# Kernel tuning notes

Hardware: AMD Instinct MI355X
Metric: run time of the kernel (lower is better)

## Reference

```python
import jax, jax.numpy as jnp
import numpy as np

B, S, HID = 2, 2048, 2048
NH, DN, DR, DV, RANK = 16, 128, 64, 128, 512
DQK = DN + DR
SCALE = DQK ** -0.5
EPS = 1e-5


def _rope(x, theta):
    # x: [..., d] with d even; theta broadcastable to [..., d//2] (angle per pair)
    x1, x2 = x[..., 0::2], x[..., 1::2]
    c, s = jnp.cos(theta), jnp.sin(theta)
    return jnp.stack([x1 * c - x2 * s, x1 * s + x2 * c], axis=-1).reshape(x.shape)


def _layernorm(x, gamma, beta):
    mu = jnp.mean(x, axis=-1, keepdims=True)
    var = jnp.var(x, axis=-1, keepdims=True)
    return (x - mu) * jax.lax.rsqrt(var + EPS) * gamma + beta


def setup_inputs() -> dict:
    key = jax.random.key(0)
    ks = jax.random.split(key, 8)
    def xavier(k, fan_in, fan_out, gain=1.0):
        lim = gain * np.sqrt(6.0 / (fan_in + fan_out))
        return jax.random.uniform(k, (fan_in, fan_out), jnp.float32, -lim, lim)
    return {
        "hidden_states": jax.random.normal(ks[0], (B, S, HID), jnp.float32),
        "freqs_cis": jax.random.uniform(ks[1], (S, DR // 2), jnp.float32) * 2.0 * np.pi,
        "Wq": xavier(ks[2], HID, NH * DQK),                      # q_proj (stored [in,out])
        "Wkv_a": xavier(ks[3], HID, RANK + DR),                  # kv_proj_a
        "kv_gamma": jnp.ones((RANK,), jnp.float32),              # kv_norm
        "kv_beta": jnp.zeros((RANK,), jnp.float32),
        "Wkv_b": xavier(ks[4], RANK, NH * (DN + DV)),            # kv_proj_b
        "Wout": xavier(ks[5], NH * DV, HID, gain=1.0 / np.sqrt(2.0)),  # out_proj
    }


def reference(hidden_states, freqs_cis, Wq, Wkv_a, kv_gamma, kv_beta, Wkv_b, Wout):
    b, s, _ = hidden_states.shape
    max_len = freqs_cis.shape[0]
    pos = jnp.arange(s) % max_len                      # [s], position_ids=None path
    theta = freqs_cis[pos]                             # [s, DR//2]

    # Q projection, split nope/rope, partial RoPE
    q = (hidden_states @ Wq).reshape(b, s, NH, DQK)
    q_nope, q_rope = q[..., :DN], q[..., DN:]
    q_rope = _rope(q_rope, theta[None, :, None, :])    # [b,s,nh,DR]

    # Low-rank KV: compressed latent + shared rope key
    kv = hidden_states @ Wkv_a                         # [b,s,RANK+DR]
    kv_c, k_rope = kv[..., :RANK], kv[..., RANK:]
    k_rope = _rope(k_rope, theta[None, :, :])          # [b,s,DR]
    kv_c = _layernorm(kv_c, kv_gamma, kv_beta)
    kvb = (kv_c @ Wkv_b).reshape(b, s, NH, DN + DV)
    k_nope, v = kvb[..., :DN], kvb[..., DN:]
    k = jnp.concatenate(
        [k_nope, jnp.broadcast_to(k_rope[:, :, None, :], (b, s, NH, DR))], axis=-1)

    q = jnp.concatenate([q_nope, q_rope], axis=-1)     # [b,s,nh,DQK]
    scores = jnp.einsum('bthd,bshd->btsh', q, k) * SCALE
    weights = jax.nn.softmax(scores.astype(jnp.float32), axis=2).astype(q.dtype)
    attn = jnp.einsum('btsh,bshd->bthd', weights, v).reshape(b, s, NH * DV)
    return attn @ Wout
```

## Files before the change

### kernel.cpp

```cpp
#include <hip/hip_runtime.h>

#define BATCH 2
#define SEQ   2048
#define HID   2048
#define NH    16
#define DN    128
#define DR    64
#define DV    128
#define RANK  512
#define DQK   192
#define NQ    (NH*DQK)
#define NKVA  576
#define NKVAP 640
#define NKVB  (NH*(DN+DV))
#define NTOK  (BATCH*SEQ)
#define SCALE_F 0.07216878364870323f

typedef __bf16 bf16x8 __attribute__((ext_vector_type(8)));
typedef float  f32x4  __attribute__((ext_vector_type(4)));
typedef unsigned int u32x4 __attribute__((ext_vector_type(4)));
typedef unsigned short u16;
typedef unsigned short u16x4 __attribute__((ext_vector_type(4)));

__device__ __forceinline__ float b2f(u16 h) {
    unsigned int u = ((unsigned int)h) << 16;
    float f; __builtin_memcpy(&f, &u, 4); return f;
}
__device__ __forceinline__ u16 f2b(float f) {
    unsigned int x; __builtin_memcpy(&x, &f, 4);
    unsigned int r = x + 0x7fffu + ((x >> 16) & 1u);
    return (u16)(r >> 16);
}
__device__ __forceinline__ bf16x8 lds_frag(const u16* p) {
    u32x4 v = *(const u32x4*)p;
    return __builtin_bit_cast(bf16x8, v);
}
__device__ __forceinline__ bf16x8 to_frag(u32x4 v) {
    return __builtin_bit_cast(bf16x8, v);
}
__device__ __forceinline__ f32x4 mfma16(bf16x8 a, bf16x8 b, f32x4 c) {
    return __builtin_amdgcn_mfma_f32_16x16x32_bf16(a, b, c, 0, 0, 0);
}
__device__ __forceinline__ void store_out(u16* p, float v) { *p = f2b(v); }
__device__ __forceinline__ void store_out(float* p, float v) { *p = v; }
__device__ __forceinline__ void gld_lds16(const u16* g, u16* l) {
    __builtin_amdgcn_global_load_lds(
        (const __attribute__((address_space(1))) unsigned int*)g,
        (__attribute__((address_space(3))) unsigned int*)l, 16, 0, 0);
}

__global__ void cast_f32_bf16(const float* __restrict__ in, u16* __restrict__ out, int n4) {
    int i = blockIdx.x * blockDim.x + threadIdx.x;
    if (i >= n4) return;
    f32x4 v = *(const f32x4*)(in + (size_t)i * 4);
    u16 o[4];
    for (int k = 0; k < 4; k++) o[k] = f2b(v[k]);
    *(unsigned long long*)(out + (size_t)i * 4) = *(unsigned long long*)o;
}

__global__ void transpose_pad(const float* __restrict__ in, u16* __restrict__ out,
                              int R, int C, int Cp) {
    __shared__ unsigned int t32[64 * 65];
    int r0 = blockIdx.x * 64, c0 = blockIdx.y * 64;
    int tid = threadIdx.x;
    bool valid = (c0 < C);
    for (int i = 0; i < 4; i++) {
        int u = tid + i * 256;
        int rl = u >> 4, c4 = u & 15;
        f32x4 v = {0.f, 0.f, 0.f, 0.f};
        if (valid) v = *(const f32x4*)&in[(size_t)(r0 + rl) * C + c0 + c4 * 4];
        for (int j = 0; j < 4; j++)
            t32[(c4 * 4 + j) * 65 + rl] = f2b(v[j]);
    }
    __syncthreads();
    for (int i = 0; i < 2; i++) {
        int u = tid + i * 256;
        int cl = u >> 3, r8 = (u & 7) * 8;
        unsigned int w[8];
        for (int j = 0; j < 8; j++) w[j] = t32[cl * 65 + r8 + j];
        u32x4 pk;
        for (int j = 0; j < 4; j++) pk[j] = (w[2 * j] & 0xffffu) | (w[2 * j + 1] << 16);
        *(u32x4*)&out[(size_t)(c0 + cl) * R + r0 + r8] = pk;
    }
}

template <typename OutT>
__global__ __launch_bounds__(256) void gemm_bt(const u16* __restrict__ A,
                                               const u16* __restrict__ Bt,
                                               OutT* __restrict__ C,
                                               int K, int lda, int ldb, int ldc) {
    __shared__ u16 As[128 * 32];
    __shared__ u16 Bs[128 * 32];
    int tid = threadIdx.x, lane = tid & 63, w = tid >> 6;
    int wm = (w >> 1) * 64, wn = (w & 1) * 64;
    int g = lane >> 4, ln = lane & 15;
    int m0 = blockIdx.y * 128, n0 = blockIdx.x * 128;
    f32x4 acc[4][4] = {};
    for (int k0 = 0; k0 < K; k0 += 32) {
        for (int i = 0; i < 2; i++) {
            int ch = tid + i * 256;
            int row = ch >> 2, o = ch & 3;
            gld_lds16(&A[(size_t)(m0 + row) * lda + k0 + o * 8], &As[row * 32 + o * 8]);
            gld_lds16(&Bt[(size_t)(n0 + row) * ldb + k0 + o * 8], &Bs[row * 32 + o * 8]);
        }
        __syncthreads();
        bf16x8 af[4], bf[4];
        for (int i = 0; i < 4; i++) af[i] = lds_frag(&As[(wm + i * 16 + ln) * 32 + g * 8]);
        for (int j = 0; j < 4; j++) bf[j] = lds_frag(&Bs[(wn + j * 16 + ln) * 32 + g * 8]);
        for (int i = 0; i < 4; i++)
            for (int j = 0; j < 4; j++)
                acc[i][j] = mfma16(af[i], bf[j], acc[i][j]);
        __syncthreads();
    }
    for (int i = 0; i < 4; i++)
        for (int j = 0; j < 4; j++)
            for (int r = 0; r < 4; r++) {
                int m = m0 + wm + i * 16 + g * 4 + r;
                int n = n0 + wn + j * 16 + ln;
                store_out(&C[(size_t)m * ldc + n], acc[i][j][r]);
            }
}

__global__ void rope_q(u16* __restrict__ q, const float* __restrict__ freqs) {
    int token = blockIdx.x;
    int s = token & (SEQ - 1);
    int tid = threadIdx.x;
    for (int i = 0; i < 2; i++) {
        int idx = tid + i * 256;
        int hh = idx >> 5, p = idx & 31;
        float th = freqs[s * 32 + p];
        float c = __cosf(th), sn = __sinf(th);
        size_t off = (size_t)token * NQ + hh * DQK + DN + 2 * p;
        float x1 = b2f(q[off]), x2 = b2f(q[off + 1]);
        q[off]     = f2b(x1 * c - x2 * sn);
        q[off + 1] = f2b(x1 * sn + x2 * c);
    }
}

__global__ void ln_kv(const u16* __restrict__ kvraw, const float* __restrict__ gamma,
                      const float* __restrict__ beta, u16* __restrict__ kv_c) {
    int row = blockIdx.x, tid = threadIdx.x;
    size_t base = (size_t)row * NKVAP;
    float x0 = b2f(kvraw[base + tid]), x1 = b2f(kvraw[base + 256 + tid]);
    float s = x0 + x1, q2 = x0 * x0 + x1 * x1;
    for (int o = 32; o > 0; o >>= 1) { s += __shfl_xor(s, o); q2 += __shfl_xor(q2, o); }
    __shared__ float sh[8];
    int lane = tid & 63, w = tid >> 6;
    if (lane == 0) { sh[w] = s; sh[4 + w] = q2; }
    __syncthreads();
    float S = sh[0] + sh[1] + sh[2] + sh[3];
    float Q2 = sh[4] + sh[5] + sh[6] + sh[7];
    float mu = S * (1.f / 512.f);
    float var = Q2 * (1.f / 512.f) - mu * mu;
    float rs = rsqrtf(var + 1e-5f);
    kv_c[(size_t)row * RANK + tid] =
        f2b((x0 - mu) * rs * gamma[tid] + beta[tid]);
    kv_c[(size_t)row * RANK + 256 + tid] =
        f2b((x1 - mu) * rs * gamma[256 + tid] + beta[256 + tid]);
}

__global__ void k_assemble(const u16* __restrict__ kvb, const u16* __restrict__ kvraw,
                           const float* __restrict__ freqs, u16* __restrict__ Kf) {
    int token = blockIdx.x;
    int s = token & (SEQ - 1);
    int tid = threadIdx.x;
    __shared__ u16 roped[64];
    if (tid < 32) {
        int p = tid;
        float th = freqs[s * 32 + p];
        float c = __cosf(th), sn = __sinf(th);
        float x1 = b2f(kvraw[(size_t)token * NKVAP + RANK + 2 * p]);
        float x2 = b2f(kvraw[(size_t)token * NKVAP + RANK + 2 * p + 1]);
        roped[2 * p]     = f2b(x1 * c - x2 * sn);
        roped[2 * p + 1] = f2b(x1 * sn + x2 * c);
    }
    __syncthreads();
    {
        int hh = tid >> 4, d8 = (tid & 15) * 8;
        *(u32x4*)&Kf[(size_t)token * NQ + hh * DQK + d8] =
            *(const u32x4*)&kvb[(size_t)token * NKVB + hh * 256 + d8];
    }
    if (tid < 128) {
        int hh = tid >> 3, d8 = (tid & 7) * 8;
        *(u32x4*)&Kf[(size_t)token * NQ + hh * DQK + DN + d8] = *(u32x4*)&roped[d8];
    }
}

__global__ void v_transpose(const u16* __restrict__ kvb, u16* __restrict__ Vt) {
    __shared__ unsigned int t32[64 * 65];
    int st = blockIdx.x * 64, dt = blockIdx.y * 64;
    int b = blockIdx.z >> 4, h = blockIdx.z & 15;
    int tid = threadIdx.x;
    for (int i = 0; i < 2; i++) {
        int u = tid + i * 256;
        int sl = u >> 3, c8 = (u & 7) * 8;
        u32x4 v = *(const u32x4*)&kvb[((size_t)(b * SEQ + st + sl) * NH + h) * 256 + DN + dt + c8];
        for (int j = 0; j < 4; j++) {
            t32[(c8 + 2 * j) * 65 + sl]     = v[j] & 0xffffu;
            t32[(c8 + 2 * j + 1) * 65 + sl] = v[j] >> 16;
        }
    }
    __syncthreads();
    for (int i = 0; i < 2; i++) {
        int u = tid + i * 256;
        int dl = u >> 3, s8 = (u & 7) * 8;
        unsigned int w[8];
        for (int j = 0; j < 8; j++) w[j] = t32[dl * 65 + s8 + j];
        u32x4 pk;
        for (int j = 0; j < 4; j++) pk[j] = (w[2 * j] & 0xffffu) | (w[2 * j + 1] << 16);
        *(u32x4*)&Vt[((size_t)(b * NH + h) * DV + dt + dl) * SEQ + st + s8] = pk;
    }
}

#define KC    64
#define QTILE 64
#define QSTR 200
#define PSTR 72
#define VSTR 72
#define NIT  (SEQ / KC)
__global__ __launch_bounds__(256, 3) void attn_kernel(const u16* __restrict__ Q,
                                                      const u16* __restrict__ Kf,
                                                      const u16* __restrict__ Vt,
                                                      u16* __restrict__ O) {
    __shared__ u16 Ks[KC * QSTR];
    __shared__ u16 Ps[QTILE * PSTR];
    __shared__ u16 Vs[DV * VSTR];
    __shared__ float lsumLDS[2][QTILE];
    int tid = threadIdx.x, lane = tid & 63, w = tid >> 6;
    int w1 = w & 1;
    int w2 = w >> 1;
    int g = lane >> 4, ln = lane & 15;
    int qt = blockIdx.x, h = blockIdx.y, b = blockIdx.z;

    size_t qbase  = ((size_t)(b * SEQ + qt * QTILE) * NH + h) * DQK;
    size_t kbase0 = ((size_t)(b * SEQ) * NH + h) * DQK;
    size_t vbase  = (size_t)(b * NH + h) * DV * SEQ;

    bf16x8 bfq[2][6];
    for (int ni = 0; ni < 2; ni++)
        for (int kk = 0; kk < 6; kk++)
            bfq[ni][kk] = to_frag(*(const u32x4*)&Q[qbase +
                (size_t)(w1 * 32 + ni * 16 + ln) * NQ + kk * 32 + g * 8]);

    u32x4 kpre[6], vpre[4];
    {
        int krow = tid >> 2;
        for (int i = 0; i < 6; i++) {
            int o = (tid & 3) + 4 * i;
            kpre[i] = *(const u32x4*)&Kf[kbase0 + (size_t)krow * NQ + o * 8];
        }
        int vrow = tid >> 1;
        for (int i = 0; i < 4; i++) {
            int o = (tid & 1) + 2 * i;
            vpre[i] = *(const u32x4*)&Vt[vbase + (size_t)vrow * SEQ + o * 8];
        }
    }
    f32x4 oacc[2][4] = {};
    float lpriv[2] = {0.f, 0.f};

    for (int kt = 0; kt < NIT; kt++) {
        {
            int krow = tid >> 2;
            for (int i = 0; i < 6; i++) {
                int o = (tid & 3) + 4 * i;
                *(u32x4*)&Ks[krow * QSTR + o * 8] = kpre[i];
            }
            int vrow = tid >> 1;
            for (int i = 0; i < 4; i++) {
                int o = (tid & 1) + 2 * i;
                *(u32x4*)&Vs[vrow * VSTR + o * 8] = vpre[i];
            }
        }
        __syncthreads();
        if (kt + 1 < NIT) {
            size_t kb = kbase0 + (size_t)(kt + 1) * KC * NQ;
            int krow = tid >> 2;
            for (int i = 0; i < 6; i++) {
                int o = (tid & 3) + 4 * i;
                kpre[i] = *(const u32x4*)&Kf[kb + (size_t)krow * NQ + o * 8];
            }
            int vrow = tid >> 1;
            int c0 = (kt + 1) * KC;
            for (int i = 0; i < 4; i++) {
                int o = (tid & 1) + 2 * i;
                vpre[i] = *(const u32x4*)&Vt[vbase + (size_t)vrow * SEQ + c0 + o * 8];
            }
        }
        f32x4 sacc[2][2] = {};
        for (int kk = 0; kk < 6; kk++) {
            bf16x8 af[2];
            for (int mi = 0; mi < 2; mi++)
                af[mi] = lds_frag(&Ks[(w2 * 32 + mi * 16 + ln) * QSTR + kk * 32 + g * 8]);
            for (int mi = 0; mi < 2; mi++)
                for (int ni = 0; ni < 2; ni++)
                    sacc[mi][ni] = mfma16(af[mi], bfq[ni][kk], sacc[mi][ni]);
        }
        for (int mi = 0; mi < 2; mi++)
            for (int ni = 0; ni < 2; ni++) {
                float p0 = __expf(sacc[mi][ni][0] * SCALE_F);
                float p1 = __expf(sacc[mi][ni][1] * SCALE_F);
                float p2 = __expf(sacc[mi][ni][2] * SCALE_F);
                float p3 = __expf(sacc[mi][ni][3] * SCALE_F);
                lpriv[ni] += (p0 + p1) + (p2 + p3);
                u16x4 pk = { f2b(p0), f2b(p1), f2b(p2), f2b(p3) };
                *(u16x4*)&Ps[(w1 * 32 + ni * 16 + ln) * PSTR + (w2 * 32 + mi * 16 + g * 4)] = pk;
            }
        __syncthreads();
        for (int kk = 0; kk < 2; kk++) {
            bf16x8 pa[2], vb[4];
            for (int mi = 0; mi < 2; mi++)
                pa[mi] = lds_frag(&Ps[(w1 * 32 + mi * 16 + ln) * PSTR + kk * 32 + g * 8]);
            for (int ni = 0; ni < 4; ni++)
                vb[ni] = lds_frag(&Vs[(w2 * 64 + ni * 16 + ln) * VSTR + kk * 32 + g * 8]);
            for (int mi = 0; mi < 2; mi++)
                for (int ni = 0; ni < 4; ni++)
                    oacc[mi][ni] = mfma16(pa[mi], vb[ni], oacc[mi][ni]);
        }
        __syncthreads();
    }

    for (int ni = 0; ni < 2; ni++) {
        float v = lpriv[ni];
        v += __shfl_xor(v, 16);
        v += __shfl_xor(v, 32);
        if (g == 0) lsumLDS[w2][w1 * 32 + ni * 16 + ln] = v;
    }
    __syncthreads();
    for (int mi = 0; mi < 2; mi++)
        for (int ni = 0; ni < 4; ni++) {
            int d = w2 * 64 + ni * 16 + ln;
            for (int r = 0; r < 4; r++) {
                int row = w1 * 32 + mi * 16 + g * 4 + r;
                float l = lsumLDS[0][row] + lsumLDS[1][row];
                O[((size_t)(b * SEQ + qt * QTILE + row) * NH + h) * DV + d] =
                    f2b(oacc[mi][ni][r] / l);
            }
        }
}

extern "C" void kernel_launch(void* const* d_in, const int* in_sizes, int n_in,
                              void* d_out, int out_size, void* d_ws, size_t ws_size,
                              hipStream_t stream) {
    const float* hs_f  = (const float*)d_in[0];
    const float* freqs = (const float*)d_in[1];
    const float* Wq    = (const float*)d_in[2];
    const float* Wkva  = (const float*)d_in[3];
    const float* gamma = (const float*)d_in[4];
    const float* beta  = (const float*)d_in[5];
    const float* Wkvb  = (const float*)d_in[6];
    const float* Wout  = (const float*)d_in[7];
    float* outp = (float*)d_out;

    char* ws = (char*)d_ws;
    size_t off = 0;
    auto alloc = [&](size_t elems) -> u16* {
        u16* p = (u16*)(ws + off);
        off += ((elems * 2 + 255) / 256) * 256;
        return p;
    };
    u16* hs    = alloc((size_t)NTOK * HID);
    u16* WqT   = alloc((size_t)NQ * HID);
    u16* WkvaT = alloc((size_t)NKVAP * HID);
    u16* WkvbT = alloc((size_t)NKVB * RANK);
    u16* WoutT = alloc((size_t)HID * HID);
    u16* q_raw = alloc((size_t)NTOK * NQ);
    u16* kvraw = alloc((size_t)NTOK * NKVAP);
    u16* kv_c  = alloc((size_t)NTOK * RANK);
    u16* kvb   = alloc((size_t)NTOK * NKVB);
    u16* Kf    = alloc((size_t)NTOK * NQ);
    u16* Vt    = alloc((size_t)BATCH * NH * DV * SEQ);
    u16* attn  = alloc((size_t)NTOK * NH * DV);
    (void)ws_size; (void)in_sizes; (void)n_in; (void)out_size;

    cast_f32_bf16<<<(NTOK * HID / 4 + 255) / 256, 256, 0, stream>>>(hs_f, hs, NTOK * HID / 4);
    transpose_pad<<<dim3(HID / 64, NQ / 64), 256, 0, stream>>>(Wq, WqT, HID, NQ, NQ);
    transpose_pad<<<dim3(HID / 64, NKVAP / 64), 256, 0, stream>>>(Wkva, WkvaT, HID, NKVA, NKVAP);
    transpose_pad<<<dim3(RANK / 64, NKVB / 64), 256, 0, stream>>>(Wkvb, WkvbT, RANK, NKVB, NKVB);
    transpose_pad<<<dim3(HID / 64, HID / 64), 256, 0, stream>>>(Wout, WoutT, HID, HID, HID);

    gemm_bt<<<dim3(NQ / 128, NTOK / 128), 256, 0, stream>>>(hs, WqT, q_raw, HID, HID, HID, NQ);
    rope_q<<<NTOK, 256, 0, stream>>>(q_raw, freqs);

    gemm_bt<<<dim3(NKVAP / 128, NTOK / 128), 256, 0, stream>>>(hs, WkvaT, kvraw, HID, HID, HID, NKVAP);
    ln_kv<<<NTOK, 256, 0, stream>>>(kvraw, gamma, beta, kv_c);

    gemm_bt<<<dim3(NKVB / 128, NTOK / 128), 256, 0, stream>>>(kv_c, WkvbT, kvb, RANK, RANK, RANK, NKVB);

    k_assemble<<<NTOK, 256, 0, stream>>>(kvb, kvraw, freqs, Kf);
    v_transpose<<<dim3(SEQ / 64, DV / 64, BATCH * NH), 256, 0, stream>>>(kvb, Vt);

    attn_kernel<<<dim3(SEQ / QTILE, NH, BATCH), 256, 0, stream>>>(q_raw, Kf, Vt, attn);

    gemm_bt<<<dim3(HID / 128, NTOK / 128), 256, 0, stream>>>(attn, WoutT, outp, HID, HID, HID, HID);
}
```

Measured before the change: 495.6 us.

## Load K via direct global-to-LDS, read V straight from global, raise occupancy

The attention kernel no longer stages K and V through registers. K tiles are copied with direct global-to-LDS loads into a fragment-ordered layout, and V fragments are read straight from global memory into registers, so the V LDS buffer and one barrier per iteration go away. Launch bounds rise from 3 to 4 blocks per CU because LDS and register use drop. In exchange, the register-level prefetch of the next tile is gone, so global load latency is less hidden. The direct LDS load issued after the last barrier also relies on the P·V phase and the next barrier for ordering, which may be racy with the Ks reads.

```diff
diff --git a/kernel.cpp b/kernel.cpp
--- a/kernel.cpp
+++ b/kernel.cpp
@@ -214,17 +214,14 @@
 
 #define KC    64
 #define QTILE 64
-#define QSTR 200
-#define PSTR 72
-#define VSTR 72
+#define PSTR  72
 #define NIT  (SEQ / KC)
-__global__ __launch_bounds__(256, 3) void attn_kernel(const u16* __restrict__ Q,
+__global__ __launch_bounds__(256, 4) void attn_kernel(const u16* __restrict__ Q,
                                                       const u16* __restrict__ Kf,
                                                       const u16* __restrict__ Vt,
                                                       u16* __restrict__ O) {
-    __shared__ u16 Ks[KC * QSTR];
+    __shared__ u16 Ks[24 * 64 * 8];
     __shared__ u16 Ps[QTILE * PSTR];
-    __shared__ u16 Vs[DV * VSTR];
     __shared__ float lsumLDS[2][QTILE];
     int tid = threadIdx.x, lane = tid & 63, w = tid >> 6;
     int w1 = w & 1;
@@ -242,55 +239,23 @@
             bfq[ni][kk] = to_frag(*(const u32x4*)&Q[qbase +
                 (size_t)(w1 * 32 + ni * 16 + ln) * NQ + kk * 32 + g * 8]);
 
-    u32x4 kpre[6], vpre[4];
-    {
-        int krow = tid >> 2;
-        for (int i = 0; i < 6; i++) {
-            int o = (tid & 3) + 4 * i;
-            kpre[i] = *(const u32x4*)&Kf[kbase0 + (size_t)krow * NQ + o * 8];
-        }
-        int vrow = tid >> 1;
-        for (int i = 0; i < 4; i++) {
-            int o = (tid & 1) + 2 * i;
-            vpre[i] = *(const u32x4*)&Vt[vbase + (size_t)vrow * SEQ + o * 8];
-        }
-    }
     f32x4 oacc[2][4] = {};
     float lpriv[2] = {0.f, 0.f};
 
     for (int kt = 0; kt < NIT; kt++) {
-        {
-            int krow = tid >> 2;
-            for (int i = 0; i < 6; i++) {
-                int o = (tid & 3) + 4 * i;
-                *(u32x4*)&Ks[krow * QSTR + o * 8] = kpre[i];
-            }
-            int vrow = tid >> 1;
-            for (int i = 0; i < 4; i++) {
-                int o = (tid & 1) + 2 * i;
-                *(u32x4*)&Vs[vrow * VSTR + o * 8] = vpre[i];
-            }
+        size_t kb = kbase0 + (size_t)kt * KC * NQ;
+        for (int i = 0; i < 6; i++) {
+            int c = tid + i * 256;
+            int r = c & 63, j = c >> 6;
+            gld_lds16(&Kf[kb + (size_t)r * NQ + j * 8], &Ks[c * 8]);
         }
         __syncthreads();
-        if (kt + 1 < NIT) {
-            size_t kb = kbase0 + (size_t)(kt + 1) * KC * NQ;
-            int krow = tid >> 2;
-            for (int i = 0; i < 6; i++) {
-                int o = (tid & 3) + 4 * i;
-                kpre[i] = *(const u32x4*)&Kf[kb + (size_t)krow * NQ + o * 8];
-            }
-            int vrow = tid >> 1;
-            int c0 = (kt + 1) * KC;
-            for (int i = 0; i < 4; i++) {
-                int o = (tid & 1) + 2 * i;
-                vpre[i] = *(const u32x4*)&Vt[vbase + (size_t)vrow * SEQ + c0 + o * 8];
-            }
-        }
+
         f32x4 sacc[2][2] = {};
         for (int kk = 0; kk < 6; kk++) {
             bf16x8 af[2];
             for (int mi = 0; mi < 2; mi++)
-                af[mi] = lds_frag(&Ks[(w2 * 32 + mi * 16 + ln) * QSTR + kk * 32 + g * 8]);
+                af[mi] = lds_frag(&Ks[(((kk * 4 + g) << 6) + w2 * 32 + mi * 16 + ln) * 8]);
             for (int mi = 0; mi < 2; mi++)
                 for (int ni = 0; ni < 2; ni++)
                     sacc[mi][ni] = mfma16(af[mi], bfq[ni][kk], sacc[mi][ni]);
@@ -305,18 +270,24 @@
                 u16x4 pk = { f2b(p0), f2b(p1), f2b(p2), f2b(p3) };
                 *(u16x4*)&Ps[(w1 * 32 + ni * 16 + ln) * PSTR + (w2 * 32 + mi * 16 + g * 4)] = pk;
             }
+        u32x4 vb[2][4];
+        {
+            int c0 = kt * KC;
+            for (int kk = 0; kk < 2; kk++)
+                for (int ni = 0; ni < 4; ni++)
+                    vb[kk][ni] = *(const u32x4*)&Vt[vbase +
+                        (size_t)(w2 * 64 + ni * 16 + ln) * SEQ + c0 + kk * 32 + g * 8];
+        }
         __syncthreads();
+
         for (int kk = 0; kk < 2; kk++) {
-            bf16x8 pa[2], vb[4];
+            bf16x8 pa[2];
             for (int mi = 0; mi < 2; mi++)
                 pa[mi] = lds_frag(&Ps[(w1 * 32 + mi * 16 + ln) * PSTR + kk * 32 + g * 8]);
-            for (int ni = 0; ni < 4; ni++)
-                vb[ni] = lds_frag(&Vs[(w2 * 64 + ni * 16 + ln) * VSTR + kk * 32 + g * 8]);
             for (int mi = 0; mi < 2; mi++)
                 for (int ni = 0; ni < 4; ni++)
-                    oacc[mi][ni] = mfma16(pa[mi], vb[ni], oacc[mi][ni]);
-        }
-        __syncthreads();
+                    oacc[mi][ni] = mfma16(pa[mi], to_frag(vb[kk][ni]), oacc[mi][ni]);
+        }
     }
 
     for (int ni = 0; ni < 2; ni++) {
```

After: 735.7 us. 1.48x slower.

## Fuse Q and KV-A projections into one GEMM and merge prep kernels

Applied to the files above, without the earlier changes.

Concatenates the transposed Wq and Wkv_a weights into a single 3712-column matrix so the Q projection and the compressed-KV projection run as one GEMM over the hidden states. The separate cast and four transpose launches are also folded into one prep kernel that dispatches by block index. Downstream kernels (rope_q, ln_kv, k_assemble, attention) now read from the combined qkv buffer with the new row stride. This is meant to cut launch overhead, read the hidden states once instead of twice, and fill the GPU better with one larger GEMM grid. The trade-off is that Q rows are no longer contiguous for the attention kernel's loads.

```diff
diff --git a/kernel.cpp b/kernel.cpp
--- a/kernel.cpp
+++ b/kernel.cpp
@@ -10,8 +10,7 @@
 #define RANK  512
 #define DQK   192
 #define NQ    (NH*DQK)
-#define NKVA  576
-#define NKVAP 640
+#define NQKV  3712
 #define NKVB  (NH*(DN+DV))
 #define NTOK  (BATCH*SEQ)
 #define SCALE_F 0.07216878364870323f
@@ -49,20 +48,29 @@
         (__attribute__((address_space(3))) unsigned int*)l, 16, 0, 0);
 }
 
-__global__ void cast_f32_bf16(const float* __restrict__ in, u16* __restrict__ out, int n4) {
-    int i = blockIdx.x * blockDim.x + threadIdx.x;
-    if (i >= n4) return;
-    f32x4 v = *(const f32x4*)(in + (size_t)i * 4);
-    u16 o[4];
-    for (int k = 0; k < 4; k++) o[k] = f2b(v[k]);
-    *(unsigned long long*)(out + (size_t)i * 4) = *(unsigned long long*)o;
-}
-
-__global__ void transpose_pad(const float* __restrict__ in, u16* __restrict__ out,
-                              int R, int C, int Cp) {
+__global__ __launch_bounds__(256) void prep_kernel(
+        const float* __restrict__ hs_f, u16* __restrict__ hs,
+        const float* __restrict__ Wq, const float* __restrict__ Wkva,
+        const float* __restrict__ Wkvb, const float* __restrict__ Wout,
+        u16* __restrict__ WqkvT, u16* __restrict__ WkvbT, u16* __restrict__ WoutT) {
+    int tid = threadIdx.x;
+    int bid = blockIdx.x;
+    if (bid < 8192) {
+        int i = bid * 256 + tid;
+        f32x4 v = *(const f32x4*)(hs_f + (size_t)i * 4);
+        u16 o[4];
+        for (int k = 0; k < 4; k++) o[k] = f2b(v[k]);
+        *(unsigned long long*)(hs + (size_t)i * 4) = *(unsigned long long*)o;
+        return;
+    }
+    bid -= 8192;
+    const float* in; u16* out; int R, C, tilesC;
+    if (bid < 1536)      { in = Wq;   out = WqkvT;                       R = HID;  C = NQ;   tilesC = 48; }
+    else if (bid < 1856) { bid -= 1536; in = Wkva; out = WqkvT + (size_t)NQ * HID; R = HID; C = 576; tilesC = 10; }
+    else if (bid < 2368) { bid -= 1856; in = Wkvb; out = WkvbT;          R = RANK; C = NKVB; tilesC = 64; }
+    else                 { bid -= 2368; in = Wout; out = WoutT;          R = HID;  C = HID;  tilesC = 32; }
     __shared__ unsigned int t32[64 * 65];
-    int r0 = blockIdx.x * 64, c0 = blockIdx.y * 64;
-    int tid = threadIdx.x;
+    int r0 = (bid / tilesC) * 64, c0 = (bid % tilesC) * 64;
     bool valid = (c0 < C);
     for (int i = 0; i < 4; i++) {
         int u = tid + i * 256;
@@ -121,7 +129,7 @@
             }
 }
 
-__global__ void rope_q(u16* __restrict__ q, const float* __restrict__ freqs) {
+__global__ void rope_q(u16* __restrict__ qkv, const float* __restrict__ freqs) {
     int token = blockIdx.x;
     int s = token & (SEQ - 1);
     int tid = threadIdx.x;
@@ -130,18 +138,18 @@
         int hh = idx >> 5, p = idx & 31;
         float th = freqs[s * 32 + p];
         float c = __cosf(th), sn = __sinf(th);
-        size_t off = (size_t)token * NQ + hh * DQK + DN + 2 * p;
-        float x1 = b2f(q[off]), x2 = b2f(q[off + 1]);
-        q[off]     = f2b(x1 * c - x2 * sn);
-        q[off + 1] = f2b(x1 * sn + x2 * c);
-    }
-}
-
-__global__ void ln_kv(const u16* __restrict__ kvraw, const float* __restrict__ gamma,
+        size_t off = (size_t)token * NQKV + hh * DQK + DN + 2 * p;
+        float x1 = b2f(qkv[off]), x2 = b2f(qkv[off + 1]);
+        qkv[off]     = f2b(x1 * c - x2 * sn);
+        qkv[off + 1] = f2b(x1 * sn + x2 * c);
+    }
+}
+
+__global__ void ln_kv(const u16* __restrict__ qkv, const float* __restrict__ gamma,
                       const float* __restrict__ beta, u16* __restrict__ kv_c) {
     int row = blockIdx.x, tid = threadIdx.x;
-    size_t base = (size_t)row * NKVAP;
-    float x0 = b2f(kvraw[base + tid]), x1 = b2f(kvraw[base + 256 + tid]);
+    size_t base = (size_t)row * NQKV + NQ;
+    float x0 = b2f(qkv[base + tid]), x1 = b2f(qkv[base + 256 + tid]);
     float s = x0 + x1, q2 = x0 * x0 + x1 * x1;
     for (int o = 32; o > 0; o >>= 1) { s += __shfl_xor(s, o); q2 += __shfl_xor(q2, o); }
     __shared__ float sh[8];
@@ -159,7 +167,7 @@
         f2b((x1 - mu) * rs * gamma[256 + tid] + beta[256 + tid]);
 }
 
-__global__ void k_assemble(const u16* __restrict__ kvb, const u16* __restrict__ kvraw,
+__global__ void k_assemble(const u16* __restrict__ kvb, const u16* __restrict__ qkv,
                            const float* __restrict__ freqs, u16* __restrict__ Kf) {
     int token = blockIdx.x;
     int s = token & (SEQ - 1);
@@ -169,8 +177,8 @@
         int p = tid;
         float th = freqs[s * 32 + p];
         float c = __cosf(th), sn = __sinf(th);
-        float x1 = b2f(kvraw[(size_t)token * NKVAP + RANK + 2 * p]);
-        float x2 = b2f(kvraw[(size_t)token * NKVAP + RANK + 2 * p + 1]);
+        float x1 = b2f(qkv[(size_t)token * NQKV + NQ + RANK + 2 * p]);
+        float x2 = b2f(qkv[(size_t)token * NQKV + NQ + RANK + 2 * p + 1]);
         roped[2 * p]     = f2b(x1 * c - x2 * sn);
         roped[2 * p + 1] = f2b(x1 * sn + x2 * c);
     }
@@ -232,7 +240,7 @@
     int g = lane >> 4, ln = lane & 15;
     int qt = blockIdx.x, h = blockIdx.y, b = blockIdx.z;
 
-    size_t qbase  = ((size_t)(b * SEQ + qt * QTILE) * NH + h) * DQK;
+    size_t qbase  = ((size_t)(b * SEQ + qt * QTILE)) * NQKV + h * DQK;
     size_t kbase0 = ((size_t)(b * SEQ) * NH + h) * DQK;
     size_t vbase  = (size_t)(b * NH + h) * DV * SEQ;
 
@@ -240,7 +248,7 @@
     for (int ni = 0; ni < 2; ni++)
         for (int kk = 0; kk < 6; kk++)
             bfq[ni][kk] = to_frag(*(const u32x4*)&Q[qbase +
-                (size_t)(w1 * 32 + ni * 16 + ln) * NQ + kk * 32 + g * 8]);
+                (size_t)(w1 * 32 + ni * 16 + ln) * NQKV + kk * 32 + g * 8]);
 
     u32x4 kpre[6], vpre[4];
     {
@@ -358,38 +366,34 @@
         off += ((elems * 2 + 255) / 256) * 256;
         return p;
     };
-    u16* hs    = alloc((size_t)NTOK * HID);
-    u16* WqT   = alloc((size_t)NQ * HID);
-    u16* WkvaT = alloc((size_t)NKVAP * HID);
-    u16* WkvbT = alloc((size_t)NKVB * RANK);
-    u16* WoutT = alloc((size_t)HID * HID);
-    u16* q_raw = alloc((size_t)NTOK * NQ);
-    u16* kvraw = alloc((size_t)NTOK * NKVAP);
-    u16* kv_c  = alloc((size_t)NTOK * RANK);
-    u16* kvb   = alloc((size_t)NTOK * NKVB);
-    u16* Kf    = alloc((size_t)NTOK * NQ);
-    u16* Vt    = alloc((size_t)BATCH * NH * DV * SEQ);
-    u16* attn  = alloc((size_t)NTOK * NH * DV);
+    u16* hs     = alloc((size_t)NTOK * HID);
+    u16* WqkvT  = alloc((size_t)NQKV * HID);
+    u16* WkvbT  = alloc((size_t)NKVB * RANK);
+    u16* WoutT  = alloc((size_t)HID * HID);
+    u16* qkv    = alloc((size_t)NTOK * NQKV);
+    u16* kv_c   = alloc((size_t)NTOK * RANK);
+    u16* kvb    = alloc((size_t)NTOK * NKVB);
+    u16* Kf     = alloc((size_t)NTOK * NQ);
+    u16* Vt     = alloc((size_t)BATCH * NH * DV * SEQ);
+    u16* attn   = alloc((size_t)NTOK * NH * DV);
     (void)ws_size; (void)in_sizes; (void)n_in; (void)out_size;
 
-    cast_f32_bf16<<<(NTOK * HID / 4 + 255) / 256, 256, 0, stream>>>(hs_f, hs, NTOK * HID / 4);
-    transpose_pad<<<dim3(HID / 64, NQ / 64), 256, 0, stream>>>(Wq, WqT, HID, NQ, NQ);
-    transpose_pad<<<dim3(HID / 64, NKVAP / 64), 256, 0, stream>>>(Wkva, WkvaT, HID, NKVA, NKVAP);
-    transpose_pad<<<dim3(RANK / 64, NKVB / 64), 256, 0, stream>>>(Wkvb, WkvbT, RANK, NKVB, NKVB);
-    transpose_pad<<<dim3(HID / 64, HID / 64), 256, 0, stream>>>(Wout, WoutT, HID, HID, HID);
-
-    gemm_bt<<<dim3(NQ / 128, NTOK / 128), 256, 0, stream>>>(hs, WqT, q_raw, HID, HID, HID, NQ);
-    rope_q<<<NTOK, 256, 0, stream>>>(q_raw, freqs);
-
-    gemm_bt<<<dim3(NKVAP / 128, NTOK / 128), 256, 0, stream>>>(hs, WkvaT, kvraw, HID, HID, HID, NKVAP);
-    ln_kv<<<NTOK, 256, 0, stream>>>(kvraw, gamma, beta, kv_c);
+    prep_kernel<<<8192 + 1536 + 320 + 512 + 1024, 256, 0, stream>>>(
+        hs_f, hs, Wq, Wkva, Wkvb, Wout, WqkvT, WkvbT, WoutT);
+
+    gemm_bt<<<dim3(NQKV / 128, NTOK / 128), 256, 0, stream>>>(hs, WqkvT, qkv, HID, HID, HID, NQKV);
+
+    rope_q<<<NTOK, 256, 0, stream>>>(qkv, freqs);
+
+    ln_kv<<<NTOK, 256, 0, stream>>>(qkv, gamma, beta, kv_c);
 
     gemm_bt<<<dim3(NKVB / 128, NTOK / 128), 256, 0, stream>>>(kv_c, WkvbT, kvb, RANK, RANK, RANK, NKVB);
 
-    k_assemble<<<NTOK, 256, 0, stream>>>(kvb, kvraw, freqs, Kf);
+    k_assemble<<<NTOK, 256, 0, stream>>>(kvb, qkv, freqs, Kf);
+
     v_transpose<<<dim3(SEQ / 64, DV / 64, BATCH * NH), 256, 0, stream>>>(kvb, Vt);
 
-    attn_kernel<<<dim3(SEQ / QTILE, NH, BATCH), 256, 0, stream>>>(q_raw, Kf, Vt, attn);
+    attn_kernel<<<dim3(SEQ / QTILE, NH, BATCH), 256, 0, stream>>>(qkv, Kf, Vt, attn);
 
     gemm_bt<<<dim3(HID / 128, NTOK / 128), 256, 0, stream>>>(attn, WoutT, outp, HID, HID, HID, HID);
 }
```

Measured after the change: 481.2 us. 2.9% less time.
